# Kernel tuning notes

Measured on AMD Instinct MI355X. Metric: run time of the kernel, lower is better.

The kernel has to match this reference:

```python
import jax, jax.numpy as jnp
import numpy as np

N = 50000   # nodes
E = 800000  # edges
G = 128     # graphs in batch
H = 128     # hidden/out dim
K = 3       # GMM kernels
L = 4       # layers
PD = 2      # pseudo_dim_MoNet
NC = 10     # classes
BN_EPS = 1e-5


def setup_inputs() -> dict:
    key = jax.random.key(0)
    ks = jax.random.split(key, 16)
    s = 1.0 / np.sqrt(H)
    inp = {
        "feature": jax.random.normal(ks[0], (N, H), jnp.float32),
        "edge_index": jax.random.randint(ks[1], (2, E), 0, N, dtype=jnp.int32),
        "batch": jnp.sort(jax.random.randint(ks[2], (N,), 0, G, dtype=jnp.int32)),
        "emb_w": jax.random.normal(ks[3], (H, H), jnp.float32) * s,
        "emb_b": jnp.zeros((H,), jnp.float32),
        "fc_w": jax.random.normal(ks[4], (L, K * H, H), jnp.float32) * s,   # per-layer GMMConv fc (no bias)
        "mu": jax.random.normal(ks[5], (L, K, PD), jnp.float32) * 0.1,
        "inv_sigma": jnp.ones((L, K, PD), jnp.float32),
        "bn_gamma": jnp.ones((L, H), jnp.float32),
        "bn_beta": jnp.zeros((L, H), jnp.float32),
        "pp_w": jax.random.normal(ks[6], (L, PD, 2), jnp.float32) * 0.7,   # pseudo_proj Linear(2, dim)
        "pp_b": jnp.zeros((L, PD), jnp.float32),
        "mlp_w0": jax.random.normal(ks[7], (H // 2, H), jnp.float32) * s,
        "mlp_b0": jnp.zeros((H // 2,), jnp.float32),
        "mlp_w1": jax.random.normal(ks[8], (H // 4, H // 2), jnp.float32) * (1.0 / np.sqrt(H // 2)),
        "mlp_b1": jnp.zeros((H // 4,), jnp.float32),
        "mlp_w2": jax.random.normal(ks[9], (NC, H // 4), jnp.float32) * (1.0 / np.sqrt(H // 4)),
        "mlp_b2": jnp.zeros((NC,), jnp.float32),
    }
    return inp


def _forward(feature, edge_index, batch, emb_w, emb_b, fc_w, mu, inv_sigma,
             bn_gamma, bn_beta, pp_w, pp_b, mlp_w0, mlp_b0, mlp_w1, mlp_b1, mlp_w2, mlp_b2):
    row, col = edge_index[0], edge_index[1]
    h = feature @ emb_w.T + emb_b                                   # [N,H]

    # degree-based pseudo coordinates (per edge)
    ones_e = jnp.ones((E,), jnp.float32)
    deg_r = jax.ops.segment_sum(ones_e, row, num_segments=N)
    deg_c = jax.ops.segment_sum(ones_e, col, num_segments=N)
    srcs = 1.0 / jnp.sqrt(deg_r[row] + 1.0)
    dsts = 1.0 / jnp.sqrt(deg_c[col] + 1.0)
    pseudo = jnp.stack([srcs, dsts], axis=-1)                        # [E,2]

    for l in range(L):
        h_in = h
        ps = jnp.tanh(pseudo @ pp_w[l].T + pp_b[l])                  # [E,PD]
        # Gaussian mixture edge weights: exp(-0.5 * sum_d ((ps-mu)^2 * inv_sigma^2))
        diff = ps[:, None, :] - mu[l][None, :, :]                    # [E,K,PD]
        w = jnp.exp(-0.5 * jnp.sum(diff * diff * (inv_sigma[l] ** 2)[None], axis=-1))  # [E,K]
        h_src = h[row]                                               # [E,H] gather
        fcl = fc_w[l].reshape(K, H, H)
        msg = jnp.zeros((E, H), h.dtype)
        for k in range(K):                                           # small fixed K, avoids [E,K,H]
            msg = msg + w[:, k:k + 1] * (h_src @ fcl[k].T)
        agg = jax.ops.segment_sum(msg, col, num_segments=N)          # scatter-add to dst [N,H]
        # batch norm (batch statistics) + ReLU + residual; dropout=0 (identity)
        mean = jnp.mean(agg, axis=0)
        var = jnp.var(agg, axis=0)
        hn = (agg - mean) * jax.lax.rsqrt(var + BN_EPS) * bn_gamma[l] + bn_beta[l]
        h = h_in + jax.nn.relu(hn)

    # mean readout over graphs
    hs = jax.ops.segment_sum(h, batch, num_segments=G)               # [G,H]
    cnt = jax.ops.segment_sum(jnp.ones((N,), jnp.float32), batch, num_segments=G)
    hg = hs / jnp.maximum(cnt, 1.0)[:, None]

    z = jax.nn.relu(hg @ mlp_w0.T + mlp_b0)
    z = jax.nn.relu(z @ mlp_w1.T + mlp_b1)
    return z @ mlp_w2.T + mlp_b2                                     # [G,NC]


def reference(feature, edge_index, batch, emb_w, emb_b, fc_w, mu, inv_sigma,
              bn_gamma, bn_beta, pp_w, pp_b, mlp_w0, mlp_b0, mlp_w1, mlp_b1, mlp_w2, mlp_b2):
    return _forward(feature, edge_index, batch, emb_w, emb_b, fc_w, mu, inv_sigma,
                    bn_gamma, bn_beta, pp_w, pp_b, mlp_w0, mlp_b0, mlp_w1, mlp_b1, mlp_w2, mlp_b2)
```

## Files before the change

kernel.cpp:

```cpp
#include <hip/hip_runtime.h>
#include <hip/hip_bf16.h>

#define N_NODES 50000
#define N_EDGES 800000
#define N_GRAPHS 128
#define HID 128
#define NK 3
#define NL 4
#define NC 10
#define BN_EPS 1e-5f
#define SCAN_G ((N_NODES + 255) / 256)
#define NSLICE 32

#define BKT_SZ 8192
#define NBKT 7
#define FP_CHK 128
#define FP_E (N_EDGES / FP_CHK)

#define H_CHK 64
#define H_E (N_EDGES / H_CHK)
#define PKW (N_NODES / 2)

typedef __attribute__((ext_vector_type(8))) _Float16 half8;
typedef __attribute__((ext_vector_type(4))) float floatx4;
typedef __attribute__((ext_vector_type(2))) float float2v;
typedef __attribute__((ext_vector_type(2))) _Float16 half2v;
typedef __attribute__((ext_vector_type(4))) _Float16 half4v;

__device__ __forceinline__ float tanh_fast(float x) {
    float ax = fabsf(x);
    float t = __expf(-2.0f * ax);
    float r = (1.0f - t) / (1.0f + t);
    return copysignf(r, x);
}

__global__ __launch_bounds__(256) void hist_lds_kernel(const int* __restrict__ row,
                                                       const int* __restrict__ col,
                                                       unsigned* __restrict__ pr,
                                                       unsigned* __restrict__ pc) {
    __shared__ unsigned hh[PKW];
    int tid = threadIdx.x;
    const int4* arr = (const int4*)(blockIdx.y ? col : row);
    unsigned* out = (blockIdx.y ? pc : pr) + (size_t)blockIdx.x * PKW;
    uint4* hh4 = (uint4*)hh;
    const uint4 z4 = {0u, 0u, 0u, 0u};
    for (int i = tid; i < PKW / 4; i += 256) hh4[i] = z4;
    __syncthreads();
    int base4 = blockIdx.x * (H_E / 4);
    for (int i = tid; i < H_E / 4; i += 256) {
        int4 v = arr[base4 + i];
        atomicAdd(&hh[v.x >> 1], 1u << ((v.x & 1) << 4));
        atomicAdd(&hh[v.y >> 1], 1u << ((v.y & 1) << 4));
        atomicAdd(&hh[v.z >> 1], 1u << ((v.z & 1) << 4));
        atomicAdd(&hh[v.w >> 1], 1u << ((v.w & 1) << 4));
    }
    __syncthreads();
    uint4* out4 = (uint4*)out;
    for (int i = tid; i < PKW / 4; i += 256) out4[i] = hh4[i];
}

__global__ __launch_bounds__(256) void hist_reduce_kernel(const unsigned* __restrict__ pr,
                                                          const unsigned* __restrict__ pc,
                                                          int* __restrict__ degr,
                                                          int* __restrict__ degc) {
    int w = blockIdx.x * 256 + threadIdx.x;
    if (w >= PKW) return;
    unsigned rlo = 0, rhi = 0, clo = 0, chi = 0;
    for (int ch = 0; ch < H_CHK; ++ch) {
        unsigned a = pr[(size_t)ch * PKW + w];
        unsigned b = pc[(size_t)ch * PKW + w];
        rlo += a & 0xFFFFu; rhi += a >> 16;
        clo += b & 0xFFFFu; chi += b >> 16;
    }
    ((int2*)degr)[w] = make_int2((int)rlo, (int)rhi);
    ((int2*)degc)[w] = make_int2((int)clo, (int)chi);
}

__global__ __launch_bounds__(256) void scan1_kernel(const int* __restrict__ degc,
                                                    int* __restrict__ csr_off,
                                                    int* __restrict__ blocksum) {
    __shared__ int buf[256];
    int tid = threadIdx.x;
    int i = blockIdx.x * 256 + tid;
    int v = (i < N_NODES) ? degc[i] : 0;
    buf[tid] = v;
    __syncthreads();
    for (int d = 1; d < 256; d <<= 1) {
        int t = (tid >= d) ? buf[tid - d] : 0;
        __syncthreads();
        buf[tid] += t;
        __syncthreads();
    }
    if (i < N_NODES) csr_off[i] = buf[tid] - v;
    if (tid == 255) blocksum[blockIdx.x] = buf[255];
}

__global__ __launch_bounds__(256) void scan2_kernel(int* __restrict__ blocksum) {
    __shared__ int buf[256];
    int tid = threadIdx.x;
    int v = (tid < SCAN_G) ? blocksum[tid] : 0;
    buf[tid] = v;
    __syncthreads();
    for (int d = 1; d < 256; d <<= 1) {
        int t = (tid >= d) ? buf[tid - d] : 0;
        __syncthreads();
        buf[tid] += t;
        __syncthreads();
    }
    if (tid < SCAN_G) blocksum[tid] = buf[tid] - v;
}

__global__ __launch_bounds__(256) void scan3_kernel(const int* __restrict__ blocksum,
                                                    int* __restrict__ csr_off,
                                                    int* __restrict__ cursor) {
    int i = blockIdx.x * 256 + threadIdx.x;
    if (i < N_NODES) {
        int v = csr_off[i] + blocksum[blockIdx.x];
        csr_off[i] = v;
        cursor[i] = v;
    }
    if (i == 0) csr_off[N_NODES] = N_EDGES;
}

__global__ __launch_bounds__(256) void fill_perm_kernel(const int* __restrict__ col,
                                                        int* __restrict__ cursor,
                                                        int* __restrict__ perm) {
    int bkt = blockIdx.x & 7;
    if (bkt >= NBKT) return;
    int chunk = blockIdx.x >> 3;
    int base = bkt * BKT_SZ;
    int e0 = chunk * FP_E;
    for (int e = e0 + threadIdx.x; e < e0 + FP_E; e += 256) {
        unsigned c = (unsigned)(col[e] - base);
        if (c < BKT_SZ) {
            int pos = atomicAdd(&cursor[base + (int)c], 1);
            perm[pos] = e;
        }
    }
}

__global__ void epack_kernel(const int* __restrict__ perm,
                             const int* __restrict__ row,
                             const int* __restrict__ degr,
                             int2* __restrict__ epack) {
    int pos = blockIdx.x * blockDim.x + threadIdx.x;
    if (pos >= N_EDGES) return;
    int e = perm[pos];
    int r = row[e];
    float px = rsqrtf((float)degr[r] + 1.0f);
    epack[pos] = make_int2(r << 8, __float_as_int(px));
}

__global__ void cvt16_dual_kernel(const float4* __restrict__ a, int n4a,
                                  const float4* __restrict__ b, int n4b,
                                  half4v* __restrict__ da, half4v* __restrict__ db) {
    int i = blockIdx.x * blockDim.x + threadIdx.x;
    const float4* src; half4v* dst; int idx;
    if (i < n4a) { src = a; dst = da; idx = i; }
    else if (i < n4a + n4b) { src = b; dst = db; idx = i - n4a; }
    else return;
    float4 f = src[idx];
    half4v o;
    o.x = (_Float16)f.x; o.y = (_Float16)f.y; o.z = (_Float16)f.z; o.w = (_Float16)f.w;
    dst[idx] = o;
}

__global__ void transpose_fc16_kernel(const float* __restrict__ fc_w,
                                      _Float16* __restrict__ w2t) {
    int idx = blockIdx.x * blockDim.x + threadIdx.x;
    if (idx >= NL * NK * HID * HID) return;
    int i = idx & (HID - 1);
    int j = (idx >> 7) & (HID - 1);
    int kl = idx >> 14;
    int k = kl % 3;
    int l = kl / 3;
    w2t[((size_t)(l * HID + j)) * (NK * HID) + k * HID + i] = (_Float16)fc_w[idx];
}

__global__ __launch_bounds__(256) void gemm_f16_kernel(
        const _Float16* __restrict__ A, const _Float16* __restrict__ W,
        const float* __restrict__ bias, _Float16* __restrict__ C16,
        float* __restrict__ bnsum, int M, int Kd) {
    __shared__ _Float16 sA[128 * 40], sB[128 * 40];
    __shared__ float bsum[HID], bsq[HID];
    int tid = threadIdx.x;
    if (bnsum && tid < HID) { bsum[tid] = 0.f; bsq[tid] = 0.f; }
    int bm = blockIdx.x * 128;
    int wave = tid >> 6, lane = tid & 63;
    int ln = lane & 15, quad = lane >> 4;
    int wy = wave >> 1, wx = wave & 1;
    int srow = tid >> 2, scol = (tid & 3) << 3;
    floatx4 acc[4][4] = {};
    const half8 zv = {0, 0, 0, 0, 0, 0, 0, 0};

    half8 pA[2], pB[2];
    bool av0 = (bm + srow) < M, av1 = (bm + srow + 64) < M;
    const size_t aoff0 = (size_t)(bm + srow) * Kd + scol;
    const size_t aoff1 = (size_t)(bm + srow + 64) * Kd + scol;
    const size_t woff0 = (size_t)srow * Kd + scol;
    const size_t woff1 = (size_t)(srow + 64) * Kd + scol;

#define LOAD_TILE(K0)                                                          \
    do {                                                                       \
        pB[0] = *(const half8*)(W + woff0 + (K0));                             \
        pB[1] = *(const half8*)(W + woff1 + (K0));                             \
        pA[0] = av0 ? *(const half8*)(A + aoff0 + (K0)) : zv;                  \
        pA[1] = av1 ? *(const half8*)(A + aoff1 + (K0)) : zv;                  \
    } while (0)

    LOAD_TILE(0);
    for (int k0 = 0; k0 < Kd; k0 += 32) {
        __syncthreads();
#pragma unroll
        for (int rep = 0; rep < 2; ++rep) {
            int r = srow + rep * 64;
            *(half8*)&sA[r * 40 + scol] = pA[rep];
            *(half8*)&sB[r * 40 + scol] = pB[rep];
        }
        __syncthreads();
        if (k0 + 32 < Kd) LOAD_TILE(k0 + 32);
        half8 a[4], b[4];
        int kq = quad * 8;
#pragma unroll
        for (int i = 0; i < 4; ++i) {
            a[i] = *(const half8*)&sA[(wy * 64 + i * 16 + ln) * 40 + kq];
            b[i] = *(const half8*)&sB[(wx * 64 + i * 16 + ln) * 40 + kq];
        }
#pragma unroll
        for (int i = 0; i < 4; ++i)
#pragma unroll
            for (int j = 0; j < 4; ++j)
                acc[i][j] = __builtin_amdgcn_mfma_f32_16x16x32_f16(a[i], b[j], acc[i][j], 0, 0, 0);
    }
#undef LOAD_TILE

#pragma unroll
    for (int j = 0; j < 4; ++j) {
        int gc = wx * 64 + j * 16 + ln;
        float bv = bias ? bias[gc] : 0.f;
#pragma unroll
        for (int i = 0; i < 4; ++i) {
#pragma unroll
            for (int r = 0; r < 4; ++r) {
                int gr = bm + wy * 64 + i * 16 + quad * 4 + r;
                if (gr < M) C16[(size_t)gr * HID + gc] = (_Float16)(acc[i][j][r] + bv);
            }
        }
    }
    if (bnsum) {
#pragma unroll
        for (int j = 0; j < 4; ++j) {
            float s = 0.f, q = 0.f;
#pragma unroll
            for (int i = 0; i < 4; ++i)
#pragma unroll
                for (int r = 0; r < 4; ++r) { float v = acc[i][j][r]; s += v; q += v * v; }
            s += __shfl_xor(s, 16); s += __shfl_xor(s, 32);
            q += __shfl_xor(q, 16); q += __shfl_xor(q, 32);
            if (quad == 0) {
                atomicAdd(&bsum[wx * 64 + j * 16 + ln], s);
                atomicAdd(&bsq[wx * 64 + j * 16 + ln], q);
            }
        }
        __syncthreads();
        float* slice = bnsum + (blockIdx.x & (NSLICE - 1)) * (2 * HID);
        if (tid < HID) {
            atomicAdd(&slice[tid],       bsum[tid]);
            atomicAdd(&slice[HID + tid], bsq[tid]);
        }
    }
}

__global__ __launch_bounds__(128) void bn_finalize_kernel(const float* __restrict__ slices,
                                                          const float* __restrict__ gamma,
                                                          const float* __restrict__ beta,
                                                          float* __restrict__ sc_sh) {
    int t = threadIdx.x;
    float s = 0.f, q = 0.f;
    for (int sl = 0; sl < NSLICE; ++sl) {
        s += slices[sl * (2 * HID) + t];
        q += slices[sl * (2 * HID) + HID + t];
    }
    const float invN = 1.0f / (float)N_NODES;
    float mean = s * invN;
    float var = q * invN - mean * mean;
    float scale = gamma[t] * rsqrtf(var + BN_EPS);
    sc_sh[t] = scale;
    sc_sh[HID + t] = beta[t] - mean * scale;
}

__global__ __launch_bounds__(256) void aggregate_kernel(const int* __restrict__ csr_off,
                                                        const int2* __restrict__ epack,
                                                        const int* __restrict__ degc,
                                                        const char* __restrict__ h16,
                                                        _Float16* __restrict__ u,
                                                        const float* __restrict__ pw,
                                                        const float* __restrict__ pb,
                                                        const float* __restrict__ mu,
                                                        const float* __restrict__ isg) {
    int wave = threadIdx.x >> 6;
    int lane = threadIdx.x & 63;
    int sub = lane >> 5;
    int sl = lane & 31;
    int base = sub << 5;
    int n = blockIdx.x * 8 + wave * 2 + sub;
    if (n >= N_NODES) return;
    int beg = csr_off[n], end = csr_off[n + 1];
    float py = rsqrtf((float)degc[n] + 1.0f);
    float pw0 = pw[0], pw1 = pw[1], pw2 = pw[2], pw3 = pw[3];
    float pb0 = pb[0], pb1 = pb[1];
    float m00 = mu[0], m01 = mu[1], m10 = mu[2], m11 = mu[3], m20 = mu[4], m21 = mu[5];
    float s00 = isg[0], s01 = isg[1], s10 = isg[2], s11 = isg[3], s20 = isg[4], s21 = isg[5];
    const char* hb = h16 + sl * 8;
    floatx4 a0 = {0.f, 0.f, 0.f, 0.f}, a1 = a0, a2 = a0;

    for (int chunk = beg; chunk < end; chunk += 32) {
        int ce = chunk + sl;
        int2 md = make_int2(0, 0);
        if (ce < end) md = epack[ce];
        float px = __int_as_float(md.y);
        float ps0 = tanh_fast(px * pw0 + py * pw1 + pb0);
        float ps1 = tanh_fast(px * pw2 + py * pw3 + pb1);
        float d0 = ps0 - m00, d1 = ps1 - m01;
        float w0 = __expf(-0.5f * (d0 * d0 * s00 * s00 + d1 * d1 * s01 * s01));
        d0 = ps0 - m10; d1 = ps1 - m11;
        float w1 = __expf(-0.5f * (d0 * d0 * s10 * s10 + d1 * d1 * s11 * s11));
        d0 = ps0 - m20; d1 = ps1 - m21;
        float w2 = __expf(-0.5f * (d0 * d0 * s20 * s20 + d1 * d1 * s21 * s21));
        int m = end - chunk; if (m > 32) m = 32;
        int t = 0;
        for (; t + 8 <= m; t += 8) {
            int ro[8];
#pragma unroll
            for (int s = 0; s < 8; ++s) ro[s] = __shfl(md.x, base + t + s);
            half4v hv[8];
#pragma unroll
            for (int s = 0; s < 8; ++s) hv[s] = *(const half4v*)(hb + (unsigned)ro[s]);
#pragma unroll
            for (int s = 0; s < 8; ++s) {
                float wx = __shfl(w0, base + t + s);
                float wy = __shfl(w1, base + t + s);
                float wz = __shfl(w2, base + t + s);
                floatx4 hf = {(float)hv[s].x, (float)hv[s].y, (float)hv[s].z, (float)hv[s].w};
                a0 += wx * hf;
                a1 += wy * hf;
                a2 += wz * hf;
            }
        }
        for (; t < m; ++t) {
            int ro = __shfl(md.x, base + t);
            float wx = __shfl(w0, base + t);
            float wy = __shfl(w1, base + t);
            float wz = __shfl(w2, base + t);
            half4v hv = *(const half4v*)(hb + (unsigned)ro);
            floatx4 hf = {(float)hv.x, (float)hv.y, (float)hv.z, (float)hv.w};
            a0 += wx * hf;
            a1 += wy * hf;
            a2 += wz * hf;
        }
    }
    size_t b = (size_t)n * 384 + sl * 4;
    half4v o0, o1, o2;
    o0.x = (_Float16)a0.x; o0.y = (_Float16)a0.y; o0.z = (_Float16)a0.z; o0.w = (_Float16)a0.w;
    o1.x = (_Float16)a1.x; o1.y = (_Float16)a1.y; o1.z = (_Float16)a1.z; o1.w = (_Float16)a1.w;
    o2.x = (_Float16)a2.x; o2.y = (_Float16)a2.y; o2.z = (_Float16)a2.z; o2.w = (_Float16)a2.w;
    *(half4v*)(u + b)       = o0;
    *(half4v*)(u + b + 128) = o1;
    *(half4v*)(u + b + 256) = o2;
}

__global__ void bn_apply_kernel(half4v* __restrict__ h16,
                                const half4v* __restrict__ agg16,
                                const float* __restrict__ sc_sh) {
    int idx = blockIdx.x * blockDim.x + threadIdx.x;
    if (idx >= N_NODES * HID / 4) return;
    int c = (idx & 31) * 4;
    half4v a = agg16[idx];
    half4v hv = h16[idx];
    half4v o16;
#pragma unroll
    for (int j = 0; j < 4; ++j) {
        float hn = (float)a[j] * sc_sh[c + j] + sc_sh[HID + c + j];
        o16[j] = (_Float16)((float)hv[j] + fmaxf(hn, 0.f));
    }
    h16[idx] = o16;
}

__global__ __launch_bounds__(1024) void readout_mlp_kernel(const _Float16* __restrict__ h16,
                                                           const int* __restrict__ batch,
                                                           const float* __restrict__ w0, const float* __restrict__ b0,
                                                           const float* __restrict__ w1, const float* __restrict__ b1,
                                                           const float* __restrict__ w2, const float* __restrict__ b2,
                                                           float* __restrict__ out) {
    __shared__ float part[8][128];
    __shared__ float hg[128];
    __shared__ float z0[64];
    __shared__ float z1[32];
    __shared__ int range[2];
    int g = blockIdx.x;
    int tid = threadIdx.x;
    if (tid == 0) {
        int lo = 0, hi = N_NODES;
        while (lo < hi) { int mid = (lo + hi) >> 1; if (batch[mid] < g) lo = mid + 1; else hi = mid; }
        range[0] = lo;
        hi = N_NODES;
        while (lo < hi) { int mid = (lo + hi) >> 1; if (batch[mid] < g + 1) lo = mid + 1; else hi = mid; }
        range[1] = lo;
    }
    __syncthreads();
    int lo = range[0], hi = range[1];
    int rg = tid >> 7;
    int ch = tid & 127;
    float s0 = 0.f, s1 = 0.f, s2 = 0.f, s3 = 0.f;
    int n = lo + rg;
    for (; n + 24 < hi; n += 32) {
        s0 += (float)h16[(size_t)n * HID + ch];
        s1 += (float)h16[(size_t)(n + 8) * HID + ch];
        s2 += (float)h16[(size_t)(n + 16) * HID + ch];
        s3 += (float)h16[(size_t)(n + 24) * HID + ch];
    }
    for (; n < hi; n += 8) s0 += (float)h16[(size_t)n * HID + ch];
    part[rg][ch] = (s0 + s1) + (s2 + s3);
    __syncthreads();
    if (tid < 128) {
        float s = 0.f;
#pragma unroll
        for (int r = 0; r < 8; ++r) s += part[r][tid];
        int cnt = hi - lo; if (cnt < 1) cnt = 1;
        hg[tid] = s / (float)cnt;
    }
    __syncthreads();
    if (tid < 64) {
        float a = b0[tid];
        for (int i = 0; i < 128; ++i) a += hg[i] * w0[tid * 128 + i];
        z0[tid] = fmaxf(a, 0.f);
    }
    __syncthreads();
    if (tid < 32) {
        float a = b1[tid];
        for (int i = 0; i < 64; ++i) a += z0[i] * w1[tid * 64 + i];
        z1[tid] = fmaxf(a, 0.f);
    }
    __syncthreads();
    if (tid < 10) {
        float a = b2[tid];
        for (int i = 0; i < 32; ++i) a += z1[i] * w2[tid * 32 + i];
        out[g * NC + tid] = a;
    }
}

extern "C" void kernel_launch(void* const* d_in, const int* in_sizes, int n_in,
                              void* d_out, int out_size, void* d_ws, size_t ws_size,
                              hipStream_t stream) {
    const float* feature = (const float*)d_in[0];
    const int*   edge    = (const int*)d_in[1];
    const int*   row     = edge;
    const int*   col     = edge + N_EDGES;
    const int*   batch   = (const int*)d_in[2];
    const float* emb_w   = (const float*)d_in[3];
    const float* emb_b   = (const float*)d_in[4];
    const float* fc_w    = (const float*)d_in[5];
    const float* mu      = (const float*)d_in[6];
    const float* isig    = (const float*)d_in[7];
    const float* gamma   = (const float*)d_in[8];
    const float* beta    = (const float*)d_in[9];
    const float* pp_w    = (const float*)d_in[10];
    const float* pp_b    = (const float*)d_in[11];
    const float* mw0     = (const float*)d_in[12];
    const float* mb0     = (const float*)d_in[13];
    const float* mw1     = (const float*)d_in[14];
    const float* mb1     = (const float*)d_in[15];
    const float* mw2     = (const float*)d_in[16];
    const float* mb2     = (const float*)d_in[17];
    float* out = (float*)d_out;

    char* ws = (char*)d_ws;
    size_t off = 0;
    auto carve = [&](size_t bytes) { size_t o = off; off = (off + bytes + 255) & ~(size_t)255; return o; };
    _Float16* h16   = (_Float16*)(ws + carve((size_t)N_NODES * HID * 2));
    _Float16* u     = (_Float16*)(ws + carve((size_t)N_NODES * NK * HID * 2));
    _Float16* agg16 = (_Float16*)(ws + carve((size_t)N_NODES * HID * 2));
    int* perm       = (int*)(ws + carve((size_t)N_EDGES * 4));
    int2* epack     = (int2*)(ws + carve((size_t)N_EDGES * 8));
    _Float16* w2t   = (_Float16*)(ws + carve((size_t)NL * HID * NK * HID * 2));
    _Float16* f16   = (_Float16*)(ws + carve((size_t)N_NODES * HID * 2));
    _Float16* e16   = (_Float16*)(ws + carve((size_t)HID * HID * 2));
    int* degr       = (int*)(ws + carve((size_t)N_NODES * 4));
    int* degc       = (int*)(ws + carve((size_t)N_NODES * 4));
    int* csr_off    = (int*)(ws + carve((size_t)(N_NODES + 1) * 4));
    int* cursor     = (int*)(ws + carve((size_t)N_NODES * 4));
    int* blocksum   = (int*)(ws + carve((size_t)SCAN_G * 4));
    unsigned* pr    = (unsigned*)(ws + carve((size_t)H_CHK * PKW * 4));
    unsigned* pc    = (unsigned*)(ws + carve((size_t)H_CHK * PKW * 4));
    float* bnsum    = (float*)(ws + carve((size_t)NL * NSLICE * 2 * HID * 4));
    float* bnfin    = (float*)(ws + carve((size_t)NL * 2 * HID * 4));
    (void)ws_size; (void)in_sizes; (void)n_in; (void)out_size;

    hipMemsetAsync(bnsum, 0, (size_t)NL * NSLICE * 2 * HID * 4, stream);

    hist_lds_kernel<<<dim3(H_CHK, 2), 256, 0, stream>>>(row, col, pr, pc);
    hist_reduce_kernel<<<(PKW + 255) / 256, 256, 0, stream>>>(pr, pc, degr, degc);
    scan1_kernel<<<SCAN_G, 256, 0, stream>>>(degc, csr_off, blocksum);
    scan2_kernel<<<1, 256, 0, stream>>>(blocksum);
    scan3_kernel<<<SCAN_G, 256, 0, stream>>>(blocksum, csr_off, cursor);
    fill_perm_kernel<<<FP_CHK * 8, 256, 0, stream>>>(col, cursor, perm);
    epack_kernel<<<(N_EDGES + 255) / 256, 256, 0, stream>>>(perm, row, degr, epack);

    cvt16_dual_kernel<<<((N_NODES * HID + HID * HID) / 4 + 255) / 256, 256, 0, stream>>>(
        (const float4*)feature, N_NODES * HID / 4, (const float4*)emb_w, HID * HID / 4,
        (half4v*)f16, (half4v*)e16);
    transpose_fc16_kernel<<<(NL * NK * HID * HID + 255) / 256, 256, 0, stream>>>(fc_w, w2t);

    gemm_f16_kernel<<<(N_NODES + 127) / 128, 256, 0, stream>>>(
        f16, e16, emb_b, h16, nullptr, N_NODES, HID);

    for (int l = 0; l < NL; ++l) {
        aggregate_kernel<<<(N_NODES + 7) / 8, 256, 0, stream>>>(
            csr_off, epack, degc, (const char*)h16, u,
            pp_w + l * 4, pp_b + l * 2, mu + l * 6, isig + l * 6);
        gemm_f16_kernel<<<(N_NODES + 127) / 128, 256, 0, stream>>>(
            u, w2t + (size_t)l * HID * NK * HID, nullptr, agg16,
            bnsum + (size_t)l * NSLICE * 2 * HID, N_NODES, NK * HID);
        bn_finalize_kernel<<<1, 128, 0, stream>>>(
            bnsum + (size_t)l * NSLICE * 2 * HID, gamma + l * HID, beta + l * HID,
            bnfin + l * 2 * HID);
        bn_apply_kernel<<<(N_NODES * HID / 4 + 255) / 256, 256, 0, stream>>>(
            (half4v*)h16, (const half4v*)agg16, bnfin + l * 2 * HID);
    }

    readout_mlp_kernel<<<N_GRAPHS, 1024, 0, stream>>>(h16, batch, mw0, mb0, mw1, mb1, mw2, mb2, out);
}
```

Before: 476.0 us.

## Fuse perm/epack and prep kernels, shrink GEMM M-tile to 64 rows

Merges the permutation fill and edge-pack kernels so each edge's packed entry is written directly at its CSR slot, which drops the intermediate perm array and one pass over it. Also merges the fp16 conversion and fc weight transpose into a single launch. The GEMM's M tile is halved from 128 to 64 rows, roughly doubling the block count on a node-heavy problem to improve occupancy and wave balance across CUs. The cost is less reuse of the W tile per block and twice as many atomic BN-statistic flushes.

```diff
diff --git a/kernel.cpp b/kernel.cpp
--- a/kernel.cpp
+++ b/kernel.cpp
@@ -122,9 +122,11 @@
     if (i == 0) csr_off[N_NODES] = N_EDGES;
 }
 
-__global__ __launch_bounds__(256) void fill_perm_kernel(const int* __restrict__ col,
-                                                        int* __restrict__ cursor,
-                                                        int* __restrict__ perm) {
+__global__ __launch_bounds__(256) void fill_epack_kernel(const int* __restrict__ col,
+                                                         const int* __restrict__ row,
+                                                         const int* __restrict__ degr,
+                                                         int* __restrict__ cursor,
+                                                         int2* __restrict__ epack) {
     int bkt = blockIdx.x & 7;
     if (bkt >= NBKT) return;
     int chunk = blockIdx.x >> 3;
@@ -134,69 +136,58 @@
         unsigned c = (unsigned)(col[e] - base);
         if (c < BKT_SZ) {
             int pos = atomicAdd(&cursor[base + (int)c], 1);
-            perm[pos] = e;
+            int r = row[e];
+            float px = rsqrtf((float)degr[r] + 1.0f);
+            epack[pos] = make_int2(r << 8, __float_as_int(px));
         }
     }
 }
 
-__global__ void epack_kernel(const int* __restrict__ perm,
-                             const int* __restrict__ row,
-                             const int* __restrict__ degr,
-                             int2* __restrict__ epack) {
-    int pos = blockIdx.x * blockDim.x + threadIdx.x;
-    if (pos >= N_EDGES) return;
-    int e = perm[pos];
-    int r = row[e];
-    float px = rsqrtf((float)degr[r] + 1.0f);
-    epack[pos] = make_int2(r << 8, __float_as_int(px));
-}
-
-__global__ void cvt16_dual_kernel(const float4* __restrict__ a, int n4a,
-                                  const float4* __restrict__ b, int n4b,
-                                  half4v* __restrict__ da, half4v* __restrict__ db) {
+__global__ void prep16_kernel(const float4* __restrict__ a, int n4a,
+                              const float4* __restrict__ b, int n4b,
+                              half4v* __restrict__ da, half4v* __restrict__ db,
+                              const float* __restrict__ fc_w,
+                              _Float16* __restrict__ w2t) {
     int i = blockIdx.x * blockDim.x + threadIdx.x;
-    const float4* src; half4v* dst; int idx;
-    if (i < n4a) { src = a; dst = da; idx = i; }
-    else if (i < n4a + n4b) { src = b; dst = db; idx = i - n4a; }
-    else return;
-    float4 f = src[idx];
-    half4v o;
-    o.x = (_Float16)f.x; o.y = (_Float16)f.y; o.z = (_Float16)f.z; o.w = (_Float16)f.w;
-    dst[idx] = o;
-}
-
-__global__ void transpose_fc16_kernel(const float* __restrict__ fc_w,
-                                      _Float16* __restrict__ w2t) {
-    int idx = blockIdx.x * blockDim.x + threadIdx.x;
+    if (i < n4a + n4b) {
+        const float4* src; half4v* dst; int idx;
+        if (i < n4a) { src = a; dst = da; idx = i; }
+        else { src = b; dst = db; idx = i - n4a; }
+        float4 f = src[idx];
+        half4v o;
+        o.x = (_Float16)f.x; o.y = (_Float16)f.y; o.z = (_Float16)f.z; o.w = (_Float16)f.w;
+        dst[idx] = o;
+        return;
+    }
+    int idx = i - (n4a + n4b);
     if (idx >= NL * NK * HID * HID) return;
-    int i = idx & (HID - 1);
+    int ii = idx & (HID - 1);
     int j = (idx >> 7) & (HID - 1);
     int kl = idx >> 14;
     int k = kl % 3;
     int l = kl / 3;
-    w2t[((size_t)(l * HID + j)) * (NK * HID) + k * HID + i] = (_Float16)fc_w[idx];
+    w2t[((size_t)(l * HID + j)) * (NK * HID) + k * HID + ii] = (_Float16)fc_w[idx];
 }
 
 __global__ __launch_bounds__(256) void gemm_f16_kernel(
         const _Float16* __restrict__ A, const _Float16* __restrict__ W,
         const float* __restrict__ bias, _Float16* __restrict__ C16,
         float* __restrict__ bnsum, int M, int Kd) {
-    __shared__ _Float16 sA[128 * 40], sB[128 * 40];
+    __shared__ _Float16 sA[64 * 40], sB[128 * 40];
     __shared__ float bsum[HID], bsq[HID];
     int tid = threadIdx.x;
     if (bnsum && tid < HID) { bsum[tid] = 0.f; bsq[tid] = 0.f; }
-    int bm = blockIdx.x * 128;
+    int bm = blockIdx.x * 64;
     int wave = tid >> 6, lane = tid & 63;
     int ln = lane & 15, quad = lane >> 4;
     int wy = wave >> 1, wx = wave & 1;
     int srow = tid >> 2, scol = (tid & 3) << 3;
-    floatx4 acc[4][4] = {};
+    floatx4 acc[2][4] = {};
     const half8 zv = {0, 0, 0, 0, 0, 0, 0, 0};
 
-    half8 pA[2], pB[2];
-    bool av0 = (bm + srow) < M, av1 = (bm + srow + 64) < M;
+    half8 pA, pB[2];
+    bool av0 = (bm + srow) < M;
     const size_t aoff0 = (size_t)(bm + srow) * Kd + scol;
-    const size_t aoff1 = (size_t)(bm + srow + 64) * Kd + scol;
     const size_t woff0 = (size_t)srow * Kd + scol;
     const size_t woff1 = (size_t)(srow + 64) * Kd + scol;
 
@@ -204,30 +195,27 @@
     do {                                                                       \
         pB[0] = *(const half8*)(W + woff0 + (K0));                             \
         pB[1] = *(const half8*)(W + woff1 + (K0));                             \
-        pA[0] = av0 ? *(const half8*)(A + aoff0 + (K0)) : zv;                  \
-        pA[1] = av1 ? *(const half8*)(A + aoff1 + (K0)) : zv;                  \
+        pA = av0 ? *(const half8*)(A + aoff0 + (K0)) : zv;                     \
     } while (0)
 
     LOAD_TILE(0);
     for (int k0 = 0; k0 < Kd; k0 += 32) {
         __syncthreads();
-#pragma unroll
-        for (int rep = 0; rep < 2; ++rep) {
-            int r = srow + rep * 64;
-            *(half8*)&sA[r * 40 + scol] = pA[rep];
-            *(half8*)&sB[r * 40 + scol] = pB[rep];
-        }
+        *(half8*)&sA[srow * 40 + scol] = pA;
+        *(half8*)&sB[srow * 40 + scol] = pB[0];
+        *(half8*)&sB[(srow + 64) * 40 + scol] = pB[1];
         __syncthreads();
         if (k0 + 32 < Kd) LOAD_TILE(k0 + 32);
-        half8 a[4], b[4];
+        half8 a[2], b[4];
         int kq = quad * 8;
 #pragma unroll
-        for (int i = 0; i < 4; ++i) {
-            a[i] = *(const half8*)&sA[(wy * 64 + i * 16 + ln) * 40 + kq];
-            b[i] = *(const half8*)&sB[(wx * 64 + i * 16 + ln) * 40 + kq];
-        }
-#pragma unroll
-        for (int i = 0; i < 4; ++i)
+        for (int i = 0; i < 2; ++i)
+            a[i] = *(const half8*)&sA[(wy * 32 + i * 16 + ln) * 40 + kq];
+#pragma unroll
+        for (int j = 0; j < 4; ++j)
+            b[j] = *(const half8*)&sB[(wx * 64 + j * 16 + ln) * 40 + kq];
+#pragma unroll
+        for (int i = 0; i < 2; ++i)
 #pragma unroll
             for (int j = 0; j < 4; ++j)
                 acc[i][j] = __builtin_amdgcn_mfma_f32_16x16x32_f16(a[i], b[j], acc[i][j], 0, 0, 0);
@@ -239,10 +227,10 @@
         int gc = wx * 64 + j * 16 + ln;
         float bv = bias ? bias[gc] : 0.f;
 #pragma unroll
-        for (int i = 0; i < 4; ++i) {
+        for (int i = 0; i < 2; ++i) {
 #pragma unroll
             for (int r = 0; r < 4; ++r) {
-                int gr = bm + wy * 64 + i * 16 + quad * 4 + r;
+                int gr = bm + wy * 32 + i * 16 + quad * 4 + r;
                 if (gr < M) C16[(size_t)gr * HID + gc] = (_Float16)(acc[i][j][r] + bv);
             }
         }
@@ -252,7 +240,7 @@
         for (int j = 0; j < 4; ++j) {
             float s = 0.f, q = 0.f;
 #pragma unroll
-            for (int i = 0; i < 4; ++i)
+            for (int i = 0; i < 2; ++i)
 #pragma unroll
                 for (int r = 0; r < 4; ++r) { float v = acc[i][j][r]; s += v; q += v * v; }
             s += __shfl_xor(s, 16); s += __shfl_xor(s, 32);
@@ -480,7 +468,6 @@
     _Float16* h16   = (_Float16*)(ws + carve((size_t)N_NODES * HID * 2));
     _Float16* u     = (_Float16*)(ws + carve((size_t)N_NODES * NK * HID * 2));
     _Float16* agg16 = (_Float16*)(ws + carve((size_t)N_NODES * HID * 2));
-    int* perm       = (int*)(ws + carve((size_t)N_EDGES * 4));
     int2* epack     = (int2*)(ws + carve((size_t)N_EDGES * 8));
     _Float16* w2t   = (_Float16*)(ws + carve((size_t)NL * HID * NK * HID * 2));
     _Float16* f16   = (_Float16*)(ws + carve((size_t)N_NODES * HID * 2));
@@ -503,22 +490,21 @@
     scan1_kernel<<<SCAN_G, 256, 0, stream>>>(degc, csr_off, blocksum);
     scan2_kernel<<<1, 256, 0, stream>>>(blocksum);
     scan3_kernel<<<SCAN_G, 256, 0, stream>>>(blocksum, csr_off, cursor);
-    fill_perm_kernel<<<FP_CHK * 8, 256, 0, stream>>>(col, cursor, perm);
-    epack_kernel<<<(N_EDGES + 255) / 256, 256, 0, stream>>>(perm, row, degr, epack);
-
-    cvt16_dual_kernel<<<((N_NODES * HID + HID * HID) / 4 + 255) / 256, 256, 0, stream>>>(
+    fill_epack_kernel<<<FP_CHK * 8, 256, 0, stream>>>(col, row, degr, cursor, epack);
+
+    prep16_kernel<<<((N_NODES * HID + HID * HID) / 4 + NL * NK * HID * HID + 255) / 256,
+                    256, 0, stream>>>(
         (const float4*)feature, N_NODES * HID / 4, (const float4*)emb_w, HID * HID / 4,
-        (half4v*)f16, (half4v*)e16);
-    transpose_fc16_kernel<<<(NL * NK * HID * HID + 255) / 256, 256, 0, stream>>>(fc_w, w2t);
-
-    gemm_f16_kernel<<<(N_NODES + 127) / 128, 256, 0, stream>>>(
+        (half4v*)f16, (half4v*)e16, fc_w, w2t);
+
+    gemm_f16_kernel<<<(N_NODES + 63) / 64, 256, 0, stream>>>(
         f16, e16, emb_b, h16, nullptr, N_NODES, HID);
 
     for (int l = 0; l < NL; ++l) {
         aggregate_kernel<<<(N_NODES + 7) / 8, 256, 0, stream>>>(
             csr_off, epack, degc, (const char*)h16, u,
             pp_w + l * 4, pp_b + l * 2, mu + l * 6, isig + l * 6);
-        gemm_f16_kernel<<<(N_NODES + 127) / 128, 256, 0, stream>>>(
+        gemm_f16_kernel<<<(N_NODES + 63) / 64, 256, 0, stream>>>(
             u, w2t + (size_t)l * HID * NK * HID, nullptr, agg16,
             bnsum + (size_t)l * NSLICE * 2 * HID, N_NODES, NK * HID);
         bn_finalize_kernel<<<1, 128, 0, stream>>>(
```

Result: faster. 454.9 us (-4.4%).
